# Kernel optimization log

Hardware: AMD Instinct MI355X
Metric: run time of the kernel (lower is better)

## Reference

```python
import jax, jax.numpy as jnp
import numpy as np

N = 50000
E = 800000
IN_C, HID_C, OUT_C = 64, 96, 32


def setup_inputs() -> dict:
    key = jax.random.key(0)
    ks = jax.random.split(key, 8)
    x = jax.random.normal(ks[0], (N, IN_C), dtype=jnp.float32)
    edge_index = jax.random.randint(ks[1], (2, E), 0, N, dtype=jnp.int32)
    W1 = jax.random.normal(ks[2], (IN_C, HID_C), dtype=jnp.float32) / np.sqrt(IN_C)
    b1 = jnp.zeros((HID_C,), jnp.float32)
    W2 = jax.random.normal(ks[3], (HID_C, HID_C), dtype=jnp.float32) / np.sqrt(HID_C)
    b2 = jnp.zeros((HID_C,), jnp.float32)
    Wfc = jax.random.normal(ks[4], (HID_C, OUT_C), dtype=jnp.float32) / np.sqrt(HID_C)
    bfc = jnp.zeros((OUT_C,), jnp.float32)
    return {"x": x, "edge_index": edge_index, "W1": W1, "b1": b1,
            "W2": W2, "b2": b2, "Wfc": Wfc, "bfc": bfc}


def _gcn_conv(x, src, dst, norm, W, b):
    # x' = D^{-1/2}(A+I)D^{-1/2} (x W) + b   (PyG GCNConv default)
    h = x @ W                                # [N, C_out]
    msg = h[src] * norm[:, None]             # gather + edge scaling
    agg = jax.ops.segment_sum(msg, dst, num_segments=N)  # scatter-add
    return agg + b


def reference(x, edge_index, W1, b1, W2, b2, Wfc, bfc):
    loop = jnp.arange(N, dtype=edge_index.dtype)
    src = jnp.concatenate([edge_index[0], loop])  # add self-loops
    dst = jnp.concatenate([edge_index[1], loop])
    deg = jax.ops.segment_sum(jnp.ones(src.shape[0], jnp.float32), dst,
                              num_segments=N)
    dinv = jax.lax.rsqrt(deg)                # deg >= 1 due to self-loops
    norm = dinv[src] * dinv[dst]             # symmetric normalization per edge
    h = jax.nn.relu(_gcn_conv(x, src, dst, norm, W1, b1))
    # dropout omitted (eval mode / identity)
    h = jax.nn.relu(_gcn_conv(h, src, dst, norm, W2, b2))
    return h @ Wfc + bfc
```

## Files before the change

kernel.cpp:

```cpp
#include <hip/hip_runtime.h>
#include <hip/hip_fp16.h>


constexpr int NN = 50000;
constexpr int NE = 800000;
constexpr int NB = 512;
constexpr int NPB = 98;
constexpr int BCAP = 2048;
constexpr int EPB = 4096;
constexpr int P1B = 256;
constexpr int NP1 = (NE + EPB - 1) / EPB;

__global__ void zero_bcnt(int* bcnt) {
  int i = threadIdx.x;
  if (i < NB) bcnt[i] = 0;
}

__global__ __launch_bounds__(P1B) void csr_pass1(const int* __restrict__ ei,
                                                 int* __restrict__ bcnt,
                                                 unsigned* __restrict__ bbuf) {
  __shared__ unsigned sorted[EPB];
  __shared__ int hist[NB];
  __shared__ int lofs[NB];
  __shared__ int cursor[NB];
  __shared__ int gbase[NB];
  __shared__ int psum[P1B];
  const int t = threadIdx.x;
  const int e0 = blockIdx.x * EPB;
  const int ecnt = min(EPB, NE - e0);

  for (int i = t; i < NB; i += P1B) hist[i] = 0;
  __syncthreads();

  for (int i = t; i < ecnt; i += P1B) {
    unsigned dst = (unsigned)ei[NE + e0 + i];
    atomicAdd(&hist[dst / NPB], 1);
  }
  __syncthreads();

  const int h0 = hist[2 * t], h1 = hist[2 * t + 1];
  psum[t] = h0 + h1;
  __syncthreads();
  for (int off = 1; off < P1B; off <<= 1) {
    int v = 0;
    if (t >= off) v = psum[t - off];
    __syncthreads();
    psum[t] += v;
    __syncthreads();
  }
  {
    const int pex = psum[t] - (h0 + h1);
    lofs[2 * t] = pex;
    lofs[2 * t + 1] = pex + h0;
    cursor[2 * t] = pex;
    cursor[2 * t + 1] = pex + h0;
    gbase[2 * t] = atomicAdd(&bcnt[2 * t], h0);
    gbase[2 * t + 1] = atomicAdd(&bcnt[2 * t + 1], h1);
  }
  __syncthreads();

  for (int i = t; i < ecnt; i += P1B) {
    unsigned src = (unsigned)ei[e0 + i];
    unsigned dst = (unsigned)ei[NE + e0 + i];
    unsigned b = dst / NPB;
    unsigned dl = dst - b * NPB;
    int pos = atomicAdd(&cursor[b], 1);
    sorted[pos] = (b << 23) | (dl << 16) | src;
  }
  __syncthreads();

  for (int i = t; i < ecnt; i += P1B) {
    unsigned pw = sorted[i];
    unsigned b = pw >> 23;
    int off_in_b = gbase[b] + (i - lofs[b]);
    if (off_in_b < BCAP)
      bbuf[b * BCAP + off_in_b] = pw & 0x007FFFFFu;
  }
}

__global__ __launch_bounds__(256) void csr_pass2(
    const int* __restrict__ bcnt, const unsigned* __restrict__ bbuf,
    const float* __restrict__ x, int* __restrict__ row_start,
    int* __restrict__ counts, float* __restrict__ dinv,
    __half* __restrict__ u, unsigned short* __restrict__ srcs,
    unsigned* __restrict__ perm) {
  __shared__ int s_red[256];
  __shared__ int s_cnt[128];
  __shared__ int s_scan[128];
  __shared__ int s_cur[128];
  __shared__ float s_dinv[128];
  __shared__ unsigned short s_sorted[BCAP];
  __shared__ int d_hist[64];
  __shared__ int d_cur[64];
  __shared__ int s_permL[NPB];
  const int b = blockIdx.x, t = threadIdx.x;
  const int cnt_b = min(bcnt[b], BCAP);

  int acc = 0;
  for (int j = t; j < b; j += 256) acc += min(bcnt[j], BCAP);
  s_red[t] = acc;
  __syncthreads();
  for (int off = 128; off > 0; off >>= 1) {
    if (t < off) s_red[t] += s_red[t + off];
    __syncthreads();
  }
  const int base = s_red[0];

  if (t < 128) s_cnt[t] = 0;
  __syncthreads();
  for (int i = t; i < cnt_b; i += 256)
    atomicAdd(&s_cnt[bbuf[b * BCAP + i] >> 16], 1);
  __syncthreads();

  if (t < 128) s_scan[t] = s_cnt[t];
  __syncthreads();
  for (int off = 1; off < 128; off <<= 1) {
    int v = 0;
    if (t < 128 && t >= off) v = s_scan[t - off];
    __syncthreads();
    if (t < 128) s_scan[t] += v;
    __syncthreads();
  }
  if (t < 128) s_cur[t] = s_scan[t] - s_cnt[t];

  const int node = b * NPB + t;
  if (t < NPB && node < NN) {
    int c = s_cnt[t];
    row_start[node] = base + s_scan[t] - c;
    counts[node] = c;
    float di = rsqrtf(1.0f + (float)c);
    dinv[node] = di;
    s_dinv[t] = di;
  }
  __syncthreads();

  for (int i = t; i < cnt_b; i += 256) {
    unsigned w = bbuf[b * BCAP + i];
    int pos = atomicAdd(&s_cur[w >> 16], 1);
    s_sorted[pos] = (unsigned short)(w & 0xFFFFu);
  }
  __syncthreads();
  for (int i = t; i < cnt_b; i += 256) srcs[base + i] = s_sorted[i];

  const int na = max(0, min(NN - b * NPB, NPB));
  if (t < 64) d_hist[t] = 0;
  __syncthreads();
  const bool activeN = (t < na);
  const int deg = activeN ? min(s_cnt[t], 63) : 0;
  if (activeN) atomicAdd(&d_hist[deg], 1);
  __syncthreads();
  if (t < 64) d_cur[t] = d_hist[t];
  __syncthreads();
  for (int off = 1; off < 64; off <<= 1) {
    int v = 0;
    if (t < 64 && t >= off) v = d_cur[t - off];
    __syncthreads();
    if (t < 64) d_cur[t] += v;
    __syncthreads();
  }
  if (t < 64) d_cur[t] -= d_hist[t];
  __syncthreads();
  if (activeN) {
    int r = atomicAdd(&d_cur[deg], 1);
    s_permL[r] = t;
  }
  __syncthreads();
  if (t < NPB)
    perm[b * NPB + t] =
        (t < na) ? (unsigned)(b * NPB + s_permL[t]) : 0xFFFFFFFFu;

  const float4* x4 = (const float4*)x;
  for (int i = t; i < NPB * 16; i += 256) {
    int nl = i >> 4, q = i & 15;
    int n = b * NPB + nl;
    if (n < NN) {
      float di = s_dinv[nl];
      float4 v = x4[(size_t)n * 16 + q];
      __half2 h01 = __floats2half2_rn(v.x * di, v.y * di);
      __half2 h23 = __floats2half2_rn(v.z * di, v.w * di);
      uint2 pk;
      pk.x = *(unsigned*)&h01;
      pk.y = *(unsigned*)&h23;
      *(uint2*)(u + (size_t)n * 64 + 4 * q) = pk;
    }
  }
}

template <int C>
__global__ __launch_bounds__(256) void gather_h(
    const unsigned* __restrict__ perm, const int* __restrict__ row_start,
    const int* __restrict__ counts, const unsigned short* __restrict__ srcs,
    const __half* __restrict__ A, float* __restrict__ B) {
  constexpr int QP = C / 8;
  int gid = blockIdx.x * blockDim.x + threadIdx.x;
  if (gid >= NB * NPB * QP) return;
  int i, q;
  if constexpr ((QP & (QP - 1)) == 0) {
    i = gid >> 3;
    q = gid & 7;
  } else {
    i = gid / QP;
    q = gid - i * QP;
  }
  const unsigned node = perm[i];
  if (node == 0xFFFFFFFFu) return;
  const int n = (int)node;
  const uint4* A4 = (const uint4*)A + q;

  float a[8] = {};
  {
    uint4 v = A4[(size_t)n * QP];
    const __half2* h = (const __half2*)&v;
    #pragma unroll
    for (int k = 0; k < 4; ++k) {
      float2 f = __half22float2(h[k]);
      a[2 * k] = f.x;
      a[2 * k + 1] = f.y;
    }
  }
  const int s0 = row_start[n];
  const int cnt = counts[n];
  int p = 0;
  for (; p + 4 <= cnt; p += 4) {
    int sa = srcs[s0 + p + 0];
    int sb = srcs[s0 + p + 1];
    int sc = srcs[s0 + p + 2];
    int sd = srcs[s0 + p + 3];
    uint4 va = A4[(size_t)sa * QP];
    uint4 vb = A4[(size_t)sb * QP];
    uint4 vc = A4[(size_t)sc * QP];
    uint4 vd = A4[(size_t)sd * QP];
    const __half2* ha = (const __half2*)&va;
    const __half2* hb = (const __half2*)&vb;
    const __half2* hc = (const __half2*)&vc;
    const __half2* hd = (const __half2*)&vd;
    #pragma unroll
    for (int k = 0; k < 4; ++k) {
      float2 fa = __half22float2(ha[k]);
      float2 fb = __half22float2(hb[k]);
      float2 fc = __half22float2(hc[k]);
      float2 fd = __half22float2(hd[k]);
      a[2 * k] += (fa.x + fb.x) + (fc.x + fd.x);
      a[2 * k + 1] += (fa.y + fb.y) + (fc.y + fd.y);
    }
  }
  for (; p < cnt; ++p) {
    int s = srcs[s0 + p];
    uint4 v = A4[(size_t)s * QP];
    const __half2* h = (const __half2*)&v;
    #pragma unroll
    for (int k = 0; k < 4; ++k) {
      float2 f = __half22float2(h[k]);
      a[2 * k] += f.x;
      a[2 * k + 1] += f.y;
    }
  }
  float* bp = B + (size_t)n * C + 8 * q;
  *(float4*)bp = make_float4(a[0], a[1], a[2], a[3]);
  *(float4*)(bp + 4) = make_float4(a[4], a[5], a[6], a[7]);
}

template <int K, int M, int MS, int EMODE, int OH>
__global__ __launch_bounds__(256) void sgemm(
    const float* __restrict__ X, const float* __restrict__ W,
    const float* __restrict__ bias, const float* __restrict__ dinv,
    void* __restrict__ outv) {
  constexpr int NS = M / MS;
  constexpr int WQ = MS / 4;
  const int bid = blockIdx.x;
  const int chunk = (NS == 1) ? bid : bid / NS;
  const int slice = (NS == 1) ? 0 : bid - chunk * NS;
  const int c0 = slice * MS;
  const int t = threadIdx.x;
  const int nr = chunk * 256 + t;
  const bool act = nr < NN;
  const int n = act ? nr : NN - 1;

  float acc[MS] = {};
  const float4* __restrict__ xr = (const float4*)(X + (size_t)n * K);
  #pragma unroll 4
  for (int kq = 0; kq < K / 4; ++kq) {
    float4 xv = xr[kq];
    const float xk[4] = {xv.x, xv.y, xv.z, xv.w};
    #pragma unroll
    for (int c = 0; c < 4; ++c) {
      const float* __restrict__ wrow = W + (size_t)(4 * kq + c) * M + c0;
      #pragma unroll
      for (int j = 0; j < MS; ++j)
        acc[j] = fmaf(xk[c], wrow[j], acc[j]);
    }
  }

  if (act) {
    const float di = (EMODE != 3) ? dinv[n] : 0.f;
    #pragma unroll
    for (int j4 = 0; j4 < WQ; ++j4) {
      float b0 = bias[c0 + 4 * j4 + 0], b1 = bias[c0 + 4 * j4 + 1];
      float b2 = bias[c0 + 4 * j4 + 2], b3 = bias[c0 + 4 * j4 + 3];
      float a0 = acc[4 * j4 + 0], a1 = acc[4 * j4 + 1];
      float a2 = acc[4 * j4 + 2], a3 = acc[4 * j4 + 3];
      float4 r;
      if (EMODE == 1) {
        r.x = di * fmaxf(fmaf(di, a0, b0), 0.f);
        r.y = di * fmaxf(fmaf(di, a1, b1), 0.f);
        r.z = di * fmaxf(fmaf(di, a2, b2), 0.f);
        r.w = di * fmaxf(fmaf(di, a3, b3), 0.f);
      } else if (EMODE == 2) {
        r.x = fmaxf(fmaf(di, a0, b0), 0.f);
        r.y = fmaxf(fmaf(di, a1, b1), 0.f);
        r.z = fmaxf(fmaf(di, a2, b2), 0.f);
        r.w = fmaxf(fmaf(di, a3, b3), 0.f);
      } else {
        r.x = a0 + b0; r.y = a1 + b1; r.z = a2 + b2; r.w = a3 + b3;
      }
      if (OH) {
        __half2 h01 = __floats2half2_rn(r.x, r.y);
        __half2 h23 = __floats2half2_rn(r.z, r.w);
        uint2 pk;
        pk.x = *(unsigned*)&h01;
        pk.y = *(unsigned*)&h23;
        *(uint2*)((__half*)outv + (size_t)n * M + c0 + 4 * j4) = pk;
      } else {
        *(float4*)((float*)outv + (size_t)n * M + c0 + 4 * j4) = r;
      }
    }
  }
}

__global__ __launch_bounds__(256) void sgemm2fc(
    const float* __restrict__ X, const float* __restrict__ W2,
    const float* __restrict__ b2, const float* __restrict__ Wfc,
    const float* __restrict__ bfc, const float* __restrict__ dinv,
    float* __restrict__ out) {
  __shared__ float sh2[64 * 101];
  const int t = threadIdx.x;
  const int nl = t & 63;
  const int c0 = __builtin_amdgcn_readfirstlane((t >> 6) * 24);
  const int nr = blockIdx.x * 64 + nl;
  const bool act = nr < NN;
  const int n = act ? nr : NN - 1;

  float acc[24] = {};
  const float4* __restrict__ xr = (const float4*)(X + (size_t)n * 96);
  #pragma unroll 4
  for (int kq = 0; kq < 24; ++kq) {
    float4 xv = xr[kq];
    const float xk[4] = {xv.x, xv.y, xv.z, xv.w};
    #pragma unroll
    for (int c = 0; c < 4; ++c) {
      const float* __restrict__ wrow = W2 + (size_t)(4 * kq + c) * 96 + c0;
      #pragma unroll
      for (int j = 0; j < 24; ++j)
        acc[j] = fmaf(xk[c], wrow[j], acc[j]);
    }
  }
  {
    const float di = dinv[n];
    float* sp = sh2 + nl * 101 + c0;
    #pragma unroll
    for (int j = 0; j < 24; ++j)
      sp[j] = fmaxf(fmaf(di, acc[j], b2[c0 + j]), 0.f);
  }
  __syncthreads();

  const int m0 = __builtin_amdgcn_readfirstlane((t >> 6) * 8);
  float o[8] = {};
  const float* __restrict__ hrow = sh2 + nl * 101;
  #pragma unroll 8
  for (int k = 0; k < 96; ++k) {
    const float hk = hrow[k];
    const float* __restrict__ wr = Wfc + (size_t)k * 32 + m0;
    #pragma unroll
    for (int j = 0; j < 8; ++j) o[j] = fmaf(hk, wr[j], o[j]);
  }
  if (act) {
    float* op = out + (size_t)nr * 32 + m0;
    float4 r0, r1;
    r0.x = o[0] + bfc[m0 + 0]; r0.y = o[1] + bfc[m0 + 1];
    r0.z = o[2] + bfc[m0 + 2]; r0.w = o[3] + bfc[m0 + 3];
    r1.x = o[4] + bfc[m0 + 4]; r1.y = o[5] + bfc[m0 + 5];
    r1.z = o[6] + bfc[m0 + 6]; r1.w = o[7] + bfc[m0 + 7];
    *(float4*)op = r0;
    *(float4*)(op + 4) = r1;
  }
}

extern "C" void kernel_launch(void* const* d_in, const int* in_sizes, int n_in,
                              void* d_out, int out_size, void* d_ws,
                              size_t ws_size, hipStream_t stream) {
  const float* x   = (const float*)d_in[0];
  const int*   ei  = (const int*)d_in[1];
  const float* W1  = (const float*)d_in[2];
  const float* b1  = (const float*)d_in[3];
  const float* W2  = (const float*)d_in[4];
  const float* b2  = (const float*)d_in[5];
  const float* Wfc = (const float*)d_in[6];
  const float* bfc = (const float*)d_in[7];
  float* out = (float*)d_out;

  float* dinv = (float*)d_ws;
  float* R0 = dinv + 50048;
  float* R1 = R0 + (size_t)NN * 96;
  int* row_start = (int*)(R1 + (size_t)NN * 96);
  int* counts = row_start + 50048;
  int* bcnt = counts + 50048;
  unsigned short* srcs = (unsigned short*)(bcnt + 512);
  unsigned* perm = (unsigned*)(srcs + NE);
  unsigned* bbuf = (unsigned*)R1;
  __half* u_h = (__half*)R0;
  __half* g1_h = (__half*)R0;
  float* B1 = R1;
  float* B2 = R1;

  zero_bcnt<<<1, 512, 0, stream>>>(bcnt);
  csr_pass1<<<NP1, P1B, 0, stream>>>(ei, bcnt, bbuf);
  csr_pass2<<<NB, 256, 0, stream>>>(bcnt, bbuf, x, row_start, counts, dinv,
                                    u_h, srcs, perm);

  constexpr int CH = (NN + 255) / 256;

  gather_h<64><<<(NB * NPB * 8 + 255) / 256, 256, 0, stream>>>(
      perm, row_start, counts, srcs, u_h, B1);
  sgemm<64, 96, 32, 1, 1><<<CH * 3, 256, 0, stream>>>(B1, W1, b1, dinv, g1_h);
  gather_h<96><<<(NB * NPB * 12 + 255) / 256, 256, 0, stream>>>(
      perm, row_start, counts, srcs, g1_h, B2);
  sgemm2fc<<<(NN + 63) / 64, 256, 0, stream>>>(B2, W2, b2, Wfc, bfc, dinv,
                                               out);
}
```

Before: 128.2 us.

## Split gathers into column slices with padded 128-wide half rows

Replaces the per-node gather with a sliced gather. Each block handles one 32-column slice of a chunk of nodes, with 4 threads per node, so the feature rows being gathered are more likely to stay in L2/L1 within a slice. The layer-1 half-precision output is padded to 128 columns (the pad is zeroed) so it divides into four equal slices, and B2 and the downstream GEMM use a 128 stride. The cost is extra memory traffic for the zero padding and redundant work on the padded slice in the second gather.

```diff
diff --git a/kernel.cpp b/kernel.cpp
--- a/kernel.cpp
+++ b/kernel.cpp
@@ -186,30 +186,30 @@
   }
 }
 
-template <int C>
-__global__ __launch_bounds__(256) void gather_h(
+template <int SLICES, int ROWH, int LDB>
+__global__ __launch_bounds__(256) void gather_slice(
     const unsigned* __restrict__ perm, const int* __restrict__ row_start,
     const int* __restrict__ counts, const unsigned short* __restrict__ srcs,
     const __half* __restrict__ A, float* __restrict__ B) {
-  constexpr int QP = C / 8;
-  int gid = blockIdx.x * blockDim.x + threadIdx.x;
-  if (gid >= NB * NPB * QP) return;
-  int i, q;
-  if constexpr ((QP & (QP - 1)) == 0) {
-    i = gid >> 3;
-    q = gid & 7;
-  } else {
-    i = gid / QP;
-    q = gid - i * QP;
-  }
+  constexpr int GPS = 8 / SLICES;
+  constexpr int NPC = 64 * GPS;
+  constexpr int RQ = ROWH / 8;
+  const int g = blockIdx.x & 7;
+  const int chunk = blockIdx.x >> 3;
+  const int slice = g / GPS;
+  const int sub = g - slice * GPS;
+  const int t = threadIdx.x;
+  const int i = chunk * NPC + sub * 64 + (t >> 2);
+  if (i >= NB * NPB) return;
   const unsigned node = perm[i];
   if (node == 0xFFFFFFFFu) return;
   const int n = (int)node;
-  const uint4* A4 = (const uint4*)A + q;
-
-  float a[8] = {};
+  const int q = t & 3;
+  const uint4* Ap = (const uint4*)A + slice * 4 + q;
+
+  float a[8];
   {
-    uint4 v = A4[(size_t)n * QP];
+    uint4 v = Ap[(size_t)n * RQ];
     const __half2* h = (const __half2*)&v;
     #pragma unroll
     for (int k = 0; k < 4; ++k) {
@@ -226,10 +226,10 @@
     int sb = srcs[s0 + p + 1];
     int sc = srcs[s0 + p + 2];
     int sd = srcs[s0 + p + 3];
-    uint4 va = A4[(size_t)sa * QP];
-    uint4 vb = A4[(size_t)sb * QP];
-    uint4 vc = A4[(size_t)sc * QP];
-    uint4 vd = A4[(size_t)sd * QP];
+    uint4 va = Ap[(size_t)sa * RQ];
+    uint4 vb = Ap[(size_t)sb * RQ];
+    uint4 vc = Ap[(size_t)sc * RQ];
+    uint4 vd = Ap[(size_t)sd * RQ];
     const __half2* ha = (const __half2*)&va;
     const __half2* hb = (const __half2*)&vb;
     const __half2* hc = (const __half2*)&vc;
@@ -246,7 +246,7 @@
   }
   for (; p < cnt; ++p) {
     int s = srcs[s0 + p];
-    uint4 v = A4[(size_t)s * QP];
+    uint4 v = Ap[(size_t)s * RQ];
     const __half2* h = (const __half2*)&v;
     #pragma unroll
     for (int k = 0; k < 4; ++k) {
@@ -255,12 +255,12 @@
       a[2 * k + 1] += f.y;
     }
   }
-  float* bp = B + (size_t)n * C + 8 * q;
+  float* bp = B + (size_t)n * LDB + slice * 32 + q * 8;
   *(float4*)bp = make_float4(a[0], a[1], a[2], a[3]);
   *(float4*)(bp + 4) = make_float4(a[4], a[5], a[6], a[7]);
 }
 
-template <int K, int M, int MS, int EMODE, int OH>
+template <int K, int M, int MS, int EMODE, int OH, int LDX, int LDO, int PADO>
 __global__ __launch_bounds__(256) void sgemm(
     const float* __restrict__ X, const float* __restrict__ W,
     const float* __restrict__ bias, const float* __restrict__ dinv,
@@ -277,7 +277,7 @@
   const int n = act ? nr : NN - 1;
 
   float acc[MS] = {};
-  const float4* __restrict__ xr = (const float4*)(X + (size_t)n * K);
+  const float4* __restrict__ xr = (const float4*)(X + (size_t)n * LDX);
   #pragma unroll 4
   for (int kq = 0; kq < K / 4; ++kq) {
     float4 xv = xr[kq];
@@ -319,10 +319,18 @@
         uint2 pk;
         pk.x = *(unsigned*)&h01;
         pk.y = *(unsigned*)&h23;
-        *(uint2*)((__half*)outv + (size_t)n * M + c0 + 4 * j4) = pk;
+        *(uint2*)((__half*)outv + (size_t)n * LDO + c0 + 4 * j4) = pk;
       } else {
-        *(float4*)((float*)outv + (size_t)n * M + c0 + 4 * j4) = r;
+        *(float4*)((float*)outv + (size_t)n * LDO + c0 + 4 * j4) = r;
       }
+    }
+    if (OH && PADO && c0 == M - MS) {
+      uint4 z = {0u, 0u, 0u, 0u};
+      __half* oh = (__half*)outv + (size_t)n * LDO + 96;
+      *(uint4*)(oh + 0) = z;
+      *(uint4*)(oh + 8) = z;
+      *(uint4*)(oh + 16) = z;
+      *(uint4*)(oh + 24) = z;
     }
   }
 }
@@ -341,7 +349,7 @@
   const int n = act ? nr : NN - 1;
 
   float acc[24] = {};
-  const float4* __restrict__ xr = (const float4*)(X + (size_t)n * 96);
+  const float4* __restrict__ xr = (const float4*)(X + (size_t)n * 128);
   #pragma unroll 4
   for (int kq = 0; kq < 24; ++kq) {
     float4 xv = xr[kq];
@@ -401,7 +409,7 @@
   float* dinv = (float*)d_ws;
   float* R0 = dinv + 50048;
   float* R1 = R0 + (size_t)NN * 96;
-  int* row_start = (int*)(R1 + (size_t)NN * 96);
+  int* row_start = (int*)(R1 + (size_t)NN * 128);
   int* counts = row_start + 50048;
   int* bcnt = counts + 50048;
   unsigned short* srcs = (unsigned short*)(bcnt + 512);
@@ -418,11 +426,14 @@
                                     u_h, srcs, perm);
 
   constexpr int CH = (NN + 255) / 256;
-
-  gather_h<64><<<(NB * NPB * 8 + 255) / 256, 256, 0, stream>>>(
-      perm, row_start, counts, srcs, u_h, B1);
-  sgemm<64, 96, 32, 1, 1><<<CH * 3, 256, 0, stream>>>(B1, W1, b1, dinv, g1_h);
-  gather_h<96><<<(NB * NPB * 12 + 255) / 256, 256, 0, stream>>>(
+  constexpr int GC2 = NB * NPB / 256;
+  constexpr int GC4 = NB * NPB / 128;
+
+  gather_slice<2, 64, 64><<<GC2 * 8, 256, 0, stream>>>(perm, row_start,
+                                                       counts, srcs, u_h, B1);
+  sgemm<64, 96, 32, 1, 1, 64, 128, 1>
+      <<<CH * 3, 256, 0, stream>>>(B1, W1, b1, dinv, g1_h);
+  gather_slice<4, 128, 128><<<GC4 * 8, 256, 0, stream>>>(
       perm, row_start, counts, srcs, g1_h, B2);
   sgemm2fc<<<(NN + 63) / 64, 256, 0, stream>>>(B2, W2, b2, Wfc, bfc, dinv,
                                                out);
```

New measurement: 152.3 us. 18.8% more time.

## Fuse neighbor gather with dense transforms into two per-layer kernels via LDS

Applied to the files above, without the earlier changes.

Each layer's sparse aggregation and its following dense GEMM now run in one kernel. A block of 64 permuted nodes gathers neighbor features into shared memory, then multiplies by W1 (layer 1) or by W2 and Wfc (layer 2) straight from LDS. This removes the fp32 intermediate buffers B1/B2, their global round trip, and two kernel launches. In exchange it uses large blocks (512/768 threads) with more LDS, and the GEMM phase follows the gather's load imbalance inside each block.

```diff
diff --git a/kernel.cpp b/kernel.cpp
--- a/kernel.cpp
+++ b/kernel.cpp
@@ -186,202 +186,215 @@
   }
 }
 
-template <int C>
-__global__ __launch_bounds__(256) void gather_h(
+__global__ __launch_bounds__(512) void gconv1(
     const unsigned* __restrict__ perm, const int* __restrict__ row_start,
     const int* __restrict__ counts, const unsigned short* __restrict__ srcs,
-    const __half* __restrict__ A, float* __restrict__ B) {
-  constexpr int QP = C / 8;
-  int gid = blockIdx.x * blockDim.x + threadIdx.x;
-  if (gid >= NB * NPB * QP) return;
-  int i, q;
-  if constexpr ((QP & (QP - 1)) == 0) {
-    i = gid >> 3;
-    q = gid & 7;
-  } else {
-    i = gid / QP;
-    q = gid - i * QP;
-  }
-  const unsigned node = perm[i];
-  if (node == 0xFFFFFFFFu) return;
-  const int n = (int)node;
-  const uint4* A4 = (const uint4*)A + q;
-
-  float a[8] = {};
+    const __half* __restrict__ u, const float* __restrict__ W1,
+    const float* __restrict__ b1, const float* __restrict__ dinv,
+    __half* __restrict__ g1) {
+  __shared__ float sh[64 * 65];
+  const int t = threadIdx.x;
+
   {
-    uint4 v = A4[(size_t)n * QP];
-    const __half2* h = (const __half2*)&v;
-    #pragma unroll
-    for (int k = 0; k < 4; ++k) {
-      float2 f = __half22float2(h[k]);
-      a[2 * k] = f.x;
-      a[2 * k + 1] = f.y;
-    }
-  }
-  const int s0 = row_start[n];
-  const int cnt = counts[n];
-  int p = 0;
-  for (; p + 4 <= cnt; p += 4) {
-    int sa = srcs[s0 + p + 0];
-    int sb = srcs[s0 + p + 1];
-    int sc = srcs[s0 + p + 2];
-    int sd = srcs[s0 + p + 3];
-    uint4 va = A4[(size_t)sa * QP];
-    uint4 vb = A4[(size_t)sb * QP];
-    uint4 vc = A4[(size_t)sc * QP];
-    uint4 vd = A4[(size_t)sd * QP];
-    const __half2* ha = (const __half2*)&va;
-    const __half2* hb = (const __half2*)&vb;
-    const __half2* hc = (const __half2*)&vc;
-    const __half2* hd = (const __half2*)&vd;
-    #pragma unroll
-    for (int k = 0; k < 4; ++k) {
-      float2 fa = __half22float2(ha[k]);
-      float2 fb = __half22float2(hb[k]);
-      float2 fc = __half22float2(hc[k]);
-      float2 fd = __half22float2(hd[k]);
-      a[2 * k] += (fa.x + fb.x) + (fc.x + fd.x);
-      a[2 * k + 1] += (fa.y + fb.y) + (fc.y + fd.y);
-    }
-  }
-  for (; p < cnt; ++p) {
-    int s = srcs[s0 + p];
-    uint4 v = A4[(size_t)s * QP];
-    const __half2* h = (const __half2*)&v;
-    #pragma unroll
-    for (int k = 0; k < 4; ++k) {
-      float2 f = __half22float2(h[k]);
-      a[2 * k] += f.x;
-      a[2 * k + 1] += f.y;
-    }
-  }
-  float* bp = B + (size_t)n * C + 8 * q;
-  *(float4*)bp = make_float4(a[0], a[1], a[2], a[3]);
-  *(float4*)(bp + 4) = make_float4(a[4], a[5], a[6], a[7]);
-}
-
-template <int K, int M, int MS, int EMODE, int OH>
-__global__ __launch_bounds__(256) void sgemm(
-    const float* __restrict__ X, const float* __restrict__ W,
-    const float* __restrict__ bias, const float* __restrict__ dinv,
-    void* __restrict__ outv) {
-  constexpr int NS = M / MS;
-  constexpr int WQ = MS / 4;
-  const int bid = blockIdx.x;
-  const int chunk = (NS == 1) ? bid : bid / NS;
-  const int slice = (NS == 1) ? 0 : bid - chunk * NS;
-  const int c0 = slice * MS;
-  const int t = threadIdx.x;
-  const int nr = chunk * 256 + t;
-  const bool act = nr < NN;
-  const int n = act ? nr : NN - 1;
-
-  float acc[MS] = {};
-  const float4* __restrict__ xr = (const float4*)(X + (size_t)n * K);
-  #pragma unroll 4
-  for (int kq = 0; kq < K / 4; ++kq) {
-    float4 xv = xr[kq];
-    const float xk[4] = {xv.x, xv.y, xv.z, xv.w};
-    #pragma unroll
-    for (int c = 0; c < 4; ++c) {
-      const float* __restrict__ wrow = W + (size_t)(4 * kq + c) * M + c0;
-      #pragma unroll
-      for (int j = 0; j < MS; ++j)
-        acc[j] = fmaf(xk[c], wrow[j], acc[j]);
-    }
-  }
-
-  if (act) {
-    const float di = (EMODE != 3) ? dinv[n] : 0.f;
-    #pragma unroll
-    for (int j4 = 0; j4 < WQ; ++j4) {
-      float b0 = bias[c0 + 4 * j4 + 0], b1 = bias[c0 + 4 * j4 + 1];
-      float b2 = bias[c0 + 4 * j4 + 2], b3 = bias[c0 + 4 * j4 + 3];
-      float a0 = acc[4 * j4 + 0], a1 = acc[4 * j4 + 1];
-      float a2 = acc[4 * j4 + 2], a3 = acc[4 * j4 + 3];
-      float4 r;
-      if (EMODE == 1) {
-        r.x = di * fmaxf(fmaf(di, a0, b0), 0.f);
-        r.y = di * fmaxf(fmaf(di, a1, b1), 0.f);
-        r.z = di * fmaxf(fmaf(di, a2, b2), 0.f);
-        r.w = di * fmaxf(fmaf(di, a3, b3), 0.f);
-      } else if (EMODE == 2) {
-        r.x = fmaxf(fmaf(di, a0, b0), 0.f);
-        r.y = fmaxf(fmaf(di, a1, b1), 0.f);
-        r.z = fmaxf(fmaf(di, a2, b2), 0.f);
-        r.w = fmaxf(fmaf(di, a3, b3), 0.f);
-      } else {
-        r.x = a0 + b0; r.y = a1 + b1; r.z = a2 + b2; r.w = a3 + b3;
-      }
-      if (OH) {
-        __half2 h01 = __floats2half2_rn(r.x, r.y);
-        __half2 h23 = __floats2half2_rn(r.z, r.w);
-        uint2 pk;
-        pk.x = *(unsigned*)&h01;
-        pk.y = *(unsigned*)&h23;
-        *(uint2*)((__half*)outv + (size_t)n * M + c0 + 4 * j4) = pk;
-      } else {
-        *(float4*)((float*)outv + (size_t)n * M + c0 + 4 * j4) = r;
-      }
-    }
-  }
-}
-
-__global__ __launch_bounds__(256) void sgemm2fc(
-    const float* __restrict__ X, const float* __restrict__ W2,
+    const int nl = t >> 3, q = t & 7;
+    const unsigned node = perm[blockIdx.x * 64 + nl];
+    if (node != 0xFFFFFFFFu) {
+      const int n = (int)node;
+      const uint4* A4 = (const uint4*)u + q;
+      float a[8];
+      {
+        uint4 v = A4[(size_t)n * 8];
+        const __half2* h = (const __half2*)&v;
+        #pragma unroll
+        for (int k = 0; k < 4; ++k) {
+          float2 f = __half22float2(h[k]);
+          a[2 * k] = f.x;
+          a[2 * k + 1] = f.y;
+        }
+      }
+      const int s0 = row_start[n];
+      const int cnt = counts[n];
+      int p = 0;
+      for (; p + 4 <= cnt; p += 4) {
+        int sa = srcs[s0 + p + 0];
+        int sb = srcs[s0 + p + 1];
+        int sc = srcs[s0 + p + 2];
+        int sd = srcs[s0 + p + 3];
+        uint4 va = A4[(size_t)sa * 8];
+        uint4 vb = A4[(size_t)sb * 8];
+        uint4 vc = A4[(size_t)sc * 8];
+        uint4 vd = A4[(size_t)sd * 8];
+        const __half2* ha = (const __half2*)&va;
+        const __half2* hb = (const __half2*)&vb;
+        const __half2* hc = (const __half2*)&vc;
+        const __half2* hd = (const __half2*)&vd;
+        #pragma unroll
+        for (int k = 0; k < 4; ++k) {
+          float2 fa = __half22float2(ha[k]);
+          float2 fb = __half22float2(hb[k]);
+          float2 fc = __half22float2(hc[k]);
+          float2 fd = __half22float2(hd[k]);
+          a[2 * k] += (fa.x + fb.x) + (fc.x + fd.x);
+          a[2 * k + 1] += (fa.y + fb.y) + (fc.y + fd.y);
+        }
+      }
+      for (; p < cnt; ++p) {
+        uint4 v = A4[(size_t)srcs[s0 + p] * 8];
+        const __half2* h = (const __half2*)&v;
+        #pragma unroll
+        for (int k = 0; k < 4; ++k) {
+          float2 f = __half22float2(h[k]);
+          a[2 * k] += f.x;
+          a[2 * k + 1] += f.y;
+        }
+      }
+      float* sp = sh + nl * 65 + q * 8;
+      #pragma unroll
+      for (int j = 0; j < 8; ++j) sp[j] = a[j];
+    }
+  }
+  __syncthreads();
+
+  {
+    const int nl = t & 63;
+    const int c0 = __builtin_amdgcn_readfirstlane((t >> 6) * 12);
+    const unsigned node = perm[blockIdx.x * 64 + nl];
+    float acc[12] = {};
+    const float* __restrict__ hrow = sh + nl * 65;
+    #pragma unroll 4
+    for (int k = 0; k < 64; ++k) {
+      const float hk = hrow[k];
+      const float* __restrict__ wrow = W1 + (size_t)k * 96 + c0;
+      #pragma unroll
+      for (int j = 0; j < 12; ++j) acc[j] = fmaf(hk, wrow[j], acc[j]);
+    }
+    if (node != 0xFFFFFFFFu) {
+      const int n = (int)node;
+      const float di = dinv[n];
+      __half* op = g1 + (size_t)n * 96 + c0;
+      #pragma unroll
+      for (int j2 = 0; j2 < 6; ++j2) {
+        float r0 = di * fmaxf(fmaf(di, acc[2 * j2 + 0], b1[c0 + 2 * j2 + 0]), 0.f);
+        float r1 = di * fmaxf(fmaf(di, acc[2 * j2 + 1], b1[c0 + 2 * j2 + 1]), 0.f);
+        __half2 h = __floats2half2_rn(r0, r1);
+        *(__half2*)(op + 2 * j2) = h;
+      }
+    }
+  }
+}
+
+__global__ __launch_bounds__(768) void gconv2(
+    const unsigned* __restrict__ perm, const int* __restrict__ row_start,
+    const int* __restrict__ counts, const unsigned short* __restrict__ srcs,
+    const __half* __restrict__ g1, const float* __restrict__ W2,
     const float* __restrict__ b2, const float* __restrict__ Wfc,
     const float* __restrict__ bfc, const float* __restrict__ dinv,
     float* __restrict__ out) {
-  __shared__ float sh2[64 * 101];
+  __shared__ float sh[64 * 97];
   const int t = threadIdx.x;
+
+  {
+    const int nl = t / 12, q = t - nl * 12;
+    const unsigned node = perm[blockIdx.x * 64 + nl];
+    if (node != 0xFFFFFFFFu) {
+      const int n = (int)node;
+      const uint4* A4 = (const uint4*)g1 + q;
+      float a[8];
+      {
+        uint4 v = A4[(size_t)n * 12];
+        const __half2* h = (const __half2*)&v;
+        #pragma unroll
+        for (int k = 0; k < 4; ++k) {
+          float2 f = __half22float2(h[k]);
+          a[2 * k] = f.x;
+          a[2 * k + 1] = f.y;
+        }
+      }
+      const int s0 = row_start[n];
+      const int cnt = counts[n];
+      int p = 0;
+      for (; p + 4 <= cnt; p += 4) {
+        int sa = srcs[s0 + p + 0];
+        int sb = srcs[s0 + p + 1];
+        int sc = srcs[s0 + p + 2];
+        int sd = srcs[s0 + p + 3];
+        uint4 va = A4[(size_t)sa * 12];
+        uint4 vb = A4[(size_t)sb * 12];
+        uint4 vc = A4[(size_t)sc * 12];
+        uint4 vd = A4[(size_t)sd * 12];
+        const __half2* ha = (const __half2*)&va;
+        const __half2* hb = (const __half2*)&vb;
+        const __half2* hc = (const __half2*)&vc;
+        const __half2* hd = (const __half2*)&vd;
+        #pragma unroll
+        for (int k = 0; k < 4; ++k) {
+          float2 fa = __half22float2(ha[k]);
+          float2 fb = __half22float2(hb[k]);
+          float2 fc = __half22float2(hc[k]);
+          float2 fd = __half22float2(hd[k]);
+          a[2 * k] += (fa.x + fb.x) + (fc.x + fd.x);
+          a[2 * k + 1] += (fa.y + fb.y) + (fc.y + fd.y);
+        }
+      }
+      for (; p < cnt; ++p) {
+        uint4 v = A4[(size_t)srcs[s0 + p] * 12];
+        const __half2* h = (const __half2*)&v;
+        #pragma unroll
+        for (int k = 0; k < 4; ++k) {
+          float2 f = __half22float2(h[k]);
+          a[2 * k] += f.x;
+          a[2 * k + 1] += f.y;
+        }
+      }
+      float* sp = sh + nl * 97 + q * 8;
+      #pragma unroll
+      for (int j = 0; j < 8; ++j) sp[j] = a[j];
+    }
+  }
+  __syncthreads();
+
   const int nl = t & 63;
-  const int c0 = __builtin_amdgcn_readfirstlane((t >> 6) * 24);
-  const int nr = blockIdx.x * 64 + nl;
-  const bool act = nr < NN;
-  const int n = act ? nr : NN - 1;
-
-  float acc[24] = {};
-  const float4* __restrict__ xr = (const float4*)(X + (size_t)n * 96);
-  #pragma unroll 4
-  for (int kq = 0; kq < 24; ++kq) {
-    float4 xv = xr[kq];
-    const float xk[4] = {xv.x, xv.y, xv.z, xv.w};
+  const unsigned node = perm[blockIdx.x * 64 + nl];
+  const int n = (node != 0xFFFFFFFFu) ? (int)node : 0;
+  float acc[8] = {};
+  {
+    const int c0 = __builtin_amdgcn_readfirstlane((t >> 6) * 8);
+    const float* __restrict__ hrow = sh + nl * 97;
+    #pragma unroll 4
+    for (int k = 0; k < 96; ++k) {
+      const float hk = hrow[k];
+      const float* __restrict__ wrow = W2 + (size_t)k * 96 + c0;
+      #pragma unroll
+      for (int j = 0; j < 8; ++j) acc[j] = fmaf(hk, wrow[j], acc[j]);
+    }
+    __syncthreads();
+    const float di = dinv[n];
+    float* sp = sh + nl * 97 + c0;
     #pragma unroll
-    for (int c = 0; c < 4; ++c) {
-      const float* __restrict__ wrow = W2 + (size_t)(4 * kq + c) * 96 + c0;
-      #pragma unroll
-      for (int j = 0; j < 24; ++j)
-        acc[j] = fmaf(xk[c], wrow[j], acc[j]);
-    }
-  }
-  {
-    const float di = dinv[n];
-    float* sp = sh2 + nl * 101 + c0;
-    #pragma unroll
-    for (int j = 0; j < 24; ++j)
+    for (int j = 0; j < 8; ++j)
       sp[j] = fmaxf(fmaf(di, acc[j], b2[c0 + j]), 0.f);
   }
   __syncthreads();
 
-  const int m0 = __builtin_amdgcn_readfirstlane((t >> 6) * 8);
-  float o[8] = {};
-  const float* __restrict__ hrow = sh2 + nl * 101;
-  #pragma unroll 8
-  for (int k = 0; k < 96; ++k) {
-    const float hk = hrow[k];
-    const float* __restrict__ wr = Wfc + (size_t)k * 32 + m0;
-    #pragma unroll
-    for (int j = 0; j < 8; ++j) o[j] = fmaf(hk, wr[j], o[j]);
-  }
-  if (act) {
-    float* op = out + (size_t)nr * 32 + m0;
-    float4 r0, r1;
-    r0.x = o[0] + bfc[m0 + 0]; r0.y = o[1] + bfc[m0 + 1];
-    r0.z = o[2] + bfc[m0 + 2]; r0.w = o[3] + bfc[m0 + 3];
-    r1.x = o[4] + bfc[m0 + 4]; r1.y = o[5] + bfc[m0 + 5];
-    r1.z = o[6] + bfc[m0 + 6]; r1.w = o[7] + bfc[m0 + 7];
-    *(float4*)op = r0;
-    *(float4*)(op + 4) = r1;
+  if (t < 512) {
+    const int m0 = __builtin_amdgcn_readfirstlane((t >> 6) * 4);
+    float o[4] = {};
+    const float* __restrict__ hrow = sh + nl * 97;
+    #pragma unroll 8
+    for (int k = 0; k < 96; ++k) {
+      const float hk = hrow[k];
+      const float* __restrict__ wr = Wfc + (size_t)k * 32 + m0;
+      #pragma unroll
+      for (int j = 0; j < 4; ++j) o[j] = fmaf(hk, wr[j], o[j]);
+    }
+    if (node != 0xFFFFFFFFu) {
+      float4 r;
+      r.x = o[0] + bfc[m0 + 0];
+      r.y = o[1] + bfc[m0 + 1];
+      r.z = o[2] + bfc[m0 + 2];
+      r.w = o[3] + bfc[m0 + 3];
+      *(float4*)(out + (size_t)n * 32 + m0) = r;
+    }
   }
 }
 
@@ -408,22 +421,17 @@
   unsigned* perm = (unsigned*)(srcs + NE);
   unsigned* bbuf = (unsigned*)R1;
   __half* u_h = (__half*)R0;
-  __half* g1_h = (__half*)R0;
-  float* B1 = R1;
-  float* B2 = R1;
+  __half* g1_h = (__half*)R1;
 
   zero_bcnt<<<1, 512, 0, stream>>>(bcnt);
   csr_pass1<<<NP1, P1B, 0, stream>>>(ei, bcnt, bbuf);
   csr_pass2<<<NB, 256, 0, stream>>>(bcnt, bbuf, x, row_start, counts, dinv,
                                     u_h, srcs, perm);
 
-  constexpr int CH = (NN + 255) / 256;
-
-  gather_h<64><<<(NB * NPB * 8 + 255) / 256, 256, 0, stream>>>(
-      perm, row_start, counts, srcs, u_h, B1);
-  sgemm<64, 96, 32, 1, 1><<<CH * 3, 256, 0, stream>>>(B1, W1, b1, dinv, g1_h);
-  gather_h<96><<<(NB * NPB * 12 + 255) / 256, 256, 0, stream>>>(
-      perm, row_start, counts, srcs, g1_h, B2);
-  sgemm2fc<<<(NN + 63) / 64, 256, 0, stream>>>(B2, W2, b2, Wfc, bfc, dinv,
-                                               out);
-}
+  constexpr int GB = NB * NPB / 64;
+
+  gconv1<<<GB, 512, 0, stream>>>(perm, row_start, counts, srcs, u_h, W1, b1,
+                                 dinv, g1_h);
+  gconv2<<<GB, 768, 0, stream>>>(perm, row_start, counts, srcs, g1_h, W2, b2,
+                                 Wfc, bfc, dinv, out);
+}
```

After: 115.8 us. -9.7%, faster.
